# Optimization experiments

Measured on AMD Instinct MI355X. Metric: run time of the kernel, lower is better.

## Reference

```python
import jax, jax.numpy as jnp
import numpy as np

B, C, H, Wd = 4, 2048, 64, 64
HID = 256


def setup_inputs() -> dict:
    key = jax.random.key(0)
    k1, k2, k3, k4 = jax.random.split(key, 4)
    return {
        "query_features": jax.random.normal(k1, (B, C, H, Wd), dtype=jnp.float32),
        "prompt_features": jax.random.normal(k2, (B, C, H, Wd), dtype=jnp.float32),
        "W": jax.random.normal(k3, (HID, C), dtype=jnp.float32) * (1.0 / np.sqrt(C)),
        "b": jax.random.normal(k4, (HID,), dtype=jnp.float32) * 0.02,
    }


def reference(query_features, prompt_features, W, b):
    # 1x1 conv == channel projection
    Q = jnp.einsum('bchw,oc->bohw', query_features, W) + b[None, :, None, None]
    K = jnp.einsum('bchw,oc->bohw', prompt_features, W) + b[None, :, None, None]
    Bq, Cf, Hq, Wq = prompt_features.shape
    V = prompt_features.reshape(Bq, Cf, Hq * Wq)              # b c p
    # full pairwise score tensor: bijkl -> b i j (k l)
    attn = jnp.einsum('bcij,bckl->bijkl', Q, K).reshape(Bq, Hq, Wq, Hq * Wq)
    attn = jax.nn.softmax(attn, axis=3)
    aligned = jnp.einsum('bijp,bcp->bcij', attn, V)           # b c h w
    return aligned
```

## Files before the change

kernel.cpp:

```cpp
#include <hip/hip_runtime.h>
#include <math.h>


#define BATCH 4
#define CH    2048
#define PP    4096
#define DD    256

typedef __bf16    bf16x8 __attribute__((ext_vector_type(8)));
typedef _Float16  f16x8  __attribute__((ext_vector_type(8)));
typedef _Float16  f16x4  __attribute__((ext_vector_type(4)));
typedef float     f32x4  __attribute__((ext_vector_type(4)));

__device__ __forceinline__ unsigned short f2bf(float f) {
  unsigned int u = __float_as_uint(f);
  unsigned int r = u + 0x7fffu + ((u >> 16) & 1u);
  return (unsigned short)(r >> 16);
}

#define GLL(src, dst) \
  __builtin_amdgcn_global_load_lds( \
      (const __attribute__((address_space(1))) unsigned int*)(uintptr_t)(src), \
      (__attribute__((address_space(3))) unsigned int*)(uintptr_t)(dst), 16, 0, 0)

__global__ __launch_bounds__(256) void prep_w(
    const float* __restrict__ W, _Float16* __restrict__ Wf) {
  int i = blockIdx.x * 256 + threadIdx.x;
  float4 v = ((const float4*)W)[i];
  f16x4 h = {(_Float16)v.x, (_Float16)v.y, (_Float16)v.z, (_Float16)v.w};
  ((f16x4*)Wf)[i] = h;
}

__global__ __launch_bounds__(256) void tsplit8(
    const float* __restrict__ Xq, const float* __restrict__ Xp,
    _Float16* __restrict__ Xt8, unsigned short* __restrict__ Vb8, int doV) {
  const int z = blockIdx.z;
  const float* __restrict__ X =
      ((z & 1) ? Xp : Xq) + (size_t)(z >> 1) * CH * PP;
  _Float16* __restrict__ Xt = Xt8 + (size_t)z * CH * PP;
  unsigned short* __restrict__ Vb = Vb8 + (size_t)(z >> 1) * CH * PP;
  const int emitV = doV & z;

  __shared__ float Ls[64 * 65];
  const int tid = threadIdx.x;
  const int pBase = blockIdx.x * 64, cBase = blockIdx.y * 64;
#pragma unroll
  for (int i = 0; i < 4; ++i) {
    int e = tid + i * 256;
    int c = e >> 4, p4 = e & 15;
    float4 v = *(const float4*)&X[(size_t)(cBase + c) * PP + pBase + p4 * 4];
    Ls[c * 65 + p4 * 4 + 0] = v.x; Ls[c * 65 + p4 * 4 + 1] = v.y;
    Ls[c * 65 + p4 * 4 + 2] = v.z; Ls[c * 65 + p4 * 4 + 3] = v.w;
    if (emitV) {
      ushort4 o;
      o.x = f2bf(v.x); o.y = f2bf(v.y); o.z = f2bf(v.z); o.w = f2bf(v.w);
      *(ushort4*)&Vb[(size_t)(cBase + c) * PP + pBase + p4 * 4] = o;
    }
  }
  __syncthreads();
#pragma unroll
  for (int j = 0; j < 4; ++j) {
    int p = (tid >> 4) + j * 16;
    int c4 = (tid & 15) * 4;
    f16x4 h = {(_Float16)Ls[(c4 + 0) * 65 + p], (_Float16)Ls[(c4 + 1) * 65 + p],
               (_Float16)Ls[(c4 + 2) * 65 + p], (_Float16)Ls[(c4 + 3) * 65 + p]};
    *(f16x4*)&Xt[(size_t)(pBase + p) * CH + cBase + c4] = h;
  }
}

__global__ __launch_bounds__(256) void proj8(
    const _Float16* __restrict__ Xt8, const _Float16* __restrict__ Wf,
    const float* __restrict__ bias,
    unsigned short* __restrict__ Qh, unsigned short* __restrict__ Ql,
    unsigned short* __restrict__ Kh, unsigned short* __restrict__ Kl) {
  const int z = blockIdx.z;
  const _Float16* __restrict__ Xt = Xt8 + (size_t)z * CH * PP;
  unsigned short* __restrict__ Yh =
      ((z & 1) ? Kh : Qh) + (size_t)(z >> 1) * PP * DD;
  unsigned short* __restrict__ Yl =
      ((z & 1) ? Kl : Ql) + (size_t)(z >> 1) * PP * DD;

  const int pBase = blockIdx.x * 64;
  const int oBase = blockIdx.y * 64;
  const int tid  = threadIdx.x;
  const int wave = tid >> 6;
  const int lane = tid & 63;
  const int wm = wave & 1, wn = wave >> 1;
  const int row16 = lane & 15, quad = lane >> 4, koff = quad * 8;

  __shared__ __align__(16) _Float16 As0[64 * 32], As1[64 * 32];
  __shared__ __align__(16) _Float16 Bs0[64 * 32], Bs1[64 * 32];

  const int sRow = lane >> 2;
  const int sKc  = (lane & 3) * 8;

  f32x4 acc[2][2];
#pragma unroll
  for (int i = 0; i < 2; ++i)
#pragma unroll
    for (int j = 0; j < 2; ++j) acc[i][j] = (f32x4){0.f, 0.f, 0.f, 0.f};

  for (int c0 = 0; c0 < CH; c0 += 64) {
    const int row = wave * 16 + sRow;
    GLL(&Xt[(size_t)(pBase + row) * CH + c0 + sKc],      &As0[(wave * 16) * 32]);
    GLL(&Xt[(size_t)(pBase + row) * CH + c0 + 32 + sKc], &As1[(wave * 16) * 32]);
    GLL(&Wf[(size_t)(oBase + row) * CH + c0 + sKc],      &Bs0[(wave * 16) * 32]);
    GLL(&Wf[(size_t)(oBase + row) * CH + c0 + 32 + sKc], &Bs1[(wave * 16) * 32]);
    __syncthreads();
#pragma unroll
    for (int s = 0; s < 2; ++s) {
      const _Float16* Ap = s ? As1 : As0;
      const _Float16* Bp = s ? Bs1 : Bs0;
      f16x8 af[2], bf[2];
#pragma unroll
      for (int i = 0; i < 2; ++i)
        af[i] = *(const f16x8*)&Ap[(wm * 32 + i * 16 + row16) * 32 + koff];
#pragma unroll
      for (int j = 0; j < 2; ++j)
        bf[j] = *(const f16x8*)&Bp[(wn * 32 + j * 16 + row16) * 32 + koff];
#pragma unroll
      for (int i = 0; i < 2; ++i)
#pragma unroll
        for (int j = 0; j < 2; ++j)
          acc[i][j] = __builtin_amdgcn_mfma_f32_16x16x32_f16(
              af[i], bf[j], acc[i][j], 0, 0, 0);
    }
    __syncthreads();
  }

#pragma unroll
  for (int i = 0; i < 2; ++i)
#pragma unroll
    for (int j = 0; j < 2; ++j) {
      const int ocol = oBase + wn * 32 + j * 16 + row16;
      const float bv = bias[ocol];
#pragma unroll
      for (int r = 0; r < 4; ++r) {
        const int prow = pBase + wm * 32 + i * 16 + quad * 4 + r;
        float y = acc[i][j][r] + bv;
        unsigned short h = f2bf(y);
        float hf = __uint_as_float((unsigned int)h << 16);
        unsigned short l = f2bf(y - hf);
        Yh[(size_t)prow * DD + ocol] = h;
        Yl[(size_t)prow * DD + ocol] = l;
      }
    }
}

__global__ __launch_bounds__(256) void softmax8(float* __restrict__ S_) {
  float* __restrict__ Sb = S_ + (size_t)blockIdx.y * PP * PP;
  unsigned short* __restrict__ Ab = (unsigned short*)Sb;
  const size_t p = blockIdx.x;
  float* row = Sb + p * PP;
  const int tid = threadIdx.x;
  float4 v[4];
#pragma unroll
  for (int i = 0; i < 4; ++i)
    v[i] = *(const float4*)&row[(i * 256 + tid) * 4];
  float m = -1e30f;
#pragma unroll
  for (int i = 0; i < 4; ++i)
    m = fmaxf(m, fmaxf(fmaxf(v[i].x, v[i].y), fmaxf(v[i].z, v[i].w)));
#pragma unroll
  for (int off = 32; off > 0; off >>= 1)
    m = fmaxf(m, __shfl_xor(m, off));
  __shared__ float red[4];
  const int lane = tid & 63, wv = tid >> 6;
  if (lane == 0) red[wv] = m;
  __syncthreads();
  m = fmaxf(fmaxf(red[0], red[1]), fmaxf(red[2], red[3]));
  __syncthreads();
  float s = 0.f;
#pragma unroll
  for (int i = 0; i < 4; ++i) {
    v[i].x = __expf(v[i].x - m);
    v[i].y = __expf(v[i].y - m);
    v[i].z = __expf(v[i].z - m);
    v[i].w = __expf(v[i].w - m);
    s += v[i].x + v[i].y + v[i].z + v[i].w;
  }
#pragma unroll
  for (int off = 32; off > 0; off >>= 1)
    s += __shfl_xor(s, off);
  if (lane == 0) red[wv] = s;
  __syncthreads();
  s = red[0] + red[1] + red[2] + red[3];
  const float inv = 1.f / s;
  unsigned short* orow = Ab + p * 8192;
#pragma unroll
  for (int i = 0; i < 4; ++i) {
    ushort4 o;
    o.x = f2bf(v[i].x * inv); o.y = f2bf(v[i].y * inv);
    o.z = f2bf(v[i].z * inv); o.w = f2bf(v[i].w * inv);
    *(ushort4*)&orow[(i * 256 + tid) * 4] = o;
  }
}

__global__ __launch_bounds__(256) void cvt_bf16(
    const float* __restrict__ X, unsigned short* __restrict__ Y, int n4) {
  int i = blockIdx.x * blockDim.x + threadIdx.x;
  if (i < n4) {
    float4 v = ((const float4*)X)[i];
    ushort4 o;
    o.x = f2bf(v.x); o.y = f2bf(v.y); o.z = f2bf(v.z); o.w = f2bf(v.w);
    ((ushort4*)Y)[i] = o;
  }
}


#define AOFF(d, h) ((d) * 32768 + (h) * 16384)
#define BOFF(d, h) (65536 + (d) * 32768 + (h) * 16384)

#define PH_READ_A(d, mh) do {                                                  \
  _Pragma("unroll")                                                            \
  for (int m_ = 0; m_ < 4; ++m_) {                                             \
    const int ro_ = AOFF(d, wm) + ((mh) * 64 + m_ * 16 + row16) * 128;         \
    aR[m_][0] = *(const bf16x8*)(Lds + ro_ + cx0);                             \
    aR[m_][1] = *(const bf16x8*)(Lds + ro_ + cx1);                             \
  } } while (0)

#define PH_READ_B(d, nh, breg) do {                                            \
  _Pragma("unroll")                                                            \
  for (int n_ = 0; n_ < 2; ++n_) {                                             \
    const int ro_ = BOFF(d, wnh) + (wnl * 64 + (nh) * 32 + n_ * 16 + row16) * 128; \
    breg[n_][0] = *(const bf16x8*)(Lds + ro_ + cx0);                           \
    breg[n_][1] = *(const bf16x8*)(Lds + ro_ + cx1);                           \
  } } while (0)

#define PH_MFMA(mh, nh, breg) do {                                             \
  __builtin_amdgcn_s_setprio(1);                                               \
  _Pragma("unroll")                                                            \
  for (int m_ = 0; m_ < 4; ++m_)                                               \
  _Pragma("unroll")                                                            \
  for (int n_ = 0; n_ < 2; ++n_) {                                             \
    f32x4 a_ = acc[(mh) * 4 + m_][(nh) * 2 + n_];                              \
    a_ = __builtin_amdgcn_mfma_f32_16x16x32_bf16(aR[m_][0], breg[n_][0], a_, 0, 0, 0); \
    a_ = __builtin_amdgcn_mfma_f32_16x16x32_bf16(aR[m_][1], breg[n_][1], a_, 0, 0, 0); \
    acc[(mh) * 4 + m_][(nh) * 2 + n_] = a_;                                    \
  }                                                                            \
  __builtin_amdgcn_s_setprio(0); } while (0)

#define PH_MFMA3(mh, nh, breg) do {                                            \
  __builtin_amdgcn_s_setprio(1);                                               \
  _Pragma("unroll")                                                            \
  for (int m_ = 0; m_ < 4; ++m_)                                               \
  _Pragma("unroll")                                                            \
  for (int n_ = 0; n_ < 2; ++n_) {                                             \
    f32x4 a_ = acc[(mh) * 4 + m_][(nh) * 2 + n_];                              \
    a_ = __builtin_amdgcn_mfma_f32_16x16x32_bf16(aR[m_][0], breg[n_][0], a_, 0, 0, 0); \
    a_ = __builtin_amdgcn_mfma_f32_16x16x32_bf16(aR[m_][0], breg[n_][1], a_, 0, 0, 0); \
    a_ = __builtin_amdgcn_mfma_f32_16x16x32_bf16(aR[m_][1], breg[n_][0], a_, 0, 0, 0); \
    acc[(mh) * 4 + m_][(nh) * 2 + n_] = a_;                                    \
  }                                                                            \
  __builtin_amdgcn_s_setprio(0); } while (0)

#define BAR_MID() do {                                                         \
  __builtin_amdgcn_sched_barrier(0);                                           \
  __builtin_amdgcn_s_barrier();                                                \
  asm volatile("s_waitcnt lgkmcnt(0)" ::: "memory");                           \
  __builtin_amdgcn_sched_barrier(0); } while (0)

#define BAR_END() __builtin_amdgcn_s_barrier()

__global__ __launch_bounds__(512, 2) void out8(
    const unsigned short* __restrict__ V_,
    const unsigned short* __restrict__ A_,
    float* __restrict__ O_) {
  const size_t z = blockIdx.z;
  const unsigned short* __restrict__ Vb = V_ + z * (size_t)CH * PP;
  const unsigned short* __restrict__ Ab = A_ + z * (size_t)PP * 8192;
  float* __restrict__ Ob = O_ + z * (size_t)CH * PP;

  const int pBase = blockIdx.x * 256;
  const int cBase = blockIdx.y * 256;
  const int tid = threadIdx.x;
  const int wave = tid >> 6, lane = tid & 63;
  const int wm = wave >> 2;
  const int wn = wave & 3;
  const int wnh = wn >> 1, wnl = wn & 1;
  const int row16 = lane & 15, quad = lane >> 4;

  __shared__ __align__(16) char Lds[131072];

  const int swz = (row16 & 7) << 4;
  const int cx0 = ((quad) << 4) ^ swz;
  const int cx1 = ((4 + quad) << 4) ^ swz;

  const int stRow0 = (wave * 2 + 0) * 8 + (lane >> 3);
  const int stRow1 = (wave * 2 + 1) * 8 + (lane >> 3);
  const int stCol  = (((lane & 7) ^ (lane >> 3)) << 4);
  char* ldsSt0 = Lds + (wave * 2 + 0) * 1024;
  char* ldsSt1 = Lds + (wave * 2 + 1) * 1024;

  const size_t VLDG = (size_t)PP * 2;
  const size_t ALDG = (size_t)8192 * 2;

  auto STG = [&](int ldsOff, const void* gbase, size_t ldgB, int rowBase, int gkB) {
    const char* g0 = (const char*)gbase + (size_t)(rowBase + stRow0) * ldgB + gkB + stCol;
    const char* g1 = (const char*)gbase + (size_t)(rowBase + stRow1) * ldgB + gkB + stCol;
    GLL(g0, ldsSt0 + ldsOff);
    GLL(g1, ldsSt1 + ldsOff);
  };

  f32x4 acc[8][4];
#pragma unroll
  for (int i = 0; i < 8; ++i)
#pragma unroll
    for (int j = 0; j < 4; ++j) acc[i][j] = (f32x4){0.f, 0.f, 0.f, 0.f};

  bf16x8 aR[4][2], bLo[2][2], bHi[2][2];

  STG(BOFF(0, 0), Ab, ALDG, pBase + 0,   0);
  STG(BOFF(0, 1), Ab, ALDG, pBase + 128, 0);
  STG(AOFF(0, 0), Vb, VLDG, cBase + 0,   0);
  STG(AOFF(0, 1), Vb, VLDG, cBase + 128, 0);
  STG(BOFF(1, 0), Ab, ALDG, pBase + 0,   128);
  STG(BOFF(1, 1), Ab, ALDG, pBase + 128, 128);
  asm volatile("s_waitcnt vmcnt(4)" ::: "memory");
  __builtin_amdgcn_s_barrier();

#pragma unroll 1
  for (int i = 0; i < 31; ++i) {
    const int t = 2 * i;
    const int gk1 = (t + 1) * 128, gk2 = (t + 2) * 128, gk3 = (t + 3) * 128;
    PH_READ_A(0, 0); PH_READ_B(0, 0, bLo);
    STG(AOFF(1, 0), Vb, VLDG, cBase + 0, gk1);
    BAR_MID(); PH_MFMA(0, 0, bLo); BAR_END();
    PH_READ_B(0, 1, bHi);
    STG(AOFF(1, 1), Vb, VLDG, cBase + 128, gk1);
    BAR_MID(); PH_MFMA(0, 1, bHi); BAR_END();
    PH_READ_A(0, 1);
    STG(BOFF(0, 0), Ab, ALDG, pBase + 0, gk2);
    BAR_MID(); PH_MFMA(1, 0, bLo); BAR_END();
    STG(BOFF(0, 1), Ab, ALDG, pBase + 128, gk2);
    BAR_MID(); PH_MFMA(1, 1, bHi);
    asm volatile("s_waitcnt vmcnt(4)" ::: "memory");
    BAR_END();
    PH_READ_A(1, 0); PH_READ_B(1, 0, bLo);
    STG(AOFF(0, 0), Vb, VLDG, cBase + 0, gk2);
    BAR_MID(); PH_MFMA(0, 0, bLo); BAR_END();
    PH_READ_B(1, 1, bHi);
    STG(AOFF(0, 1), Vb, VLDG, cBase + 128, gk2);
    BAR_MID(); PH_MFMA(0, 1, bHi); BAR_END();
    PH_READ_A(1, 1);
    STG(BOFF(1, 0), Ab, ALDG, pBase + 0, gk3);
    BAR_MID(); PH_MFMA(1, 0, bLo); BAR_END();
    STG(BOFF(1, 1), Ab, ALDG, pBase + 128, gk3);
    BAR_MID(); PH_MFMA(1, 1, bHi);
    asm volatile("s_waitcnt vmcnt(4)" ::: "memory");
    BAR_END();
  }

  {
    const int gk1 = 63 * 128;
    PH_READ_A(0, 0); PH_READ_B(0, 0, bLo);
    STG(AOFF(1, 0), Vb, VLDG, cBase + 0, gk1);
    BAR_MID(); PH_MFMA(0, 0, bLo); BAR_END();
    PH_READ_B(0, 1, bHi);
    STG(AOFF(1, 1), Vb, VLDG, cBase + 128, gk1);
    BAR_MID(); PH_MFMA(0, 1, bHi); BAR_END();
    PH_READ_A(0, 1);
    BAR_MID(); PH_MFMA(1, 0, bLo); BAR_END();
    BAR_MID(); PH_MFMA(1, 1, bHi);
    asm volatile("s_waitcnt vmcnt(0)" ::: "memory");
    BAR_END();
    PH_READ_A(1, 0); PH_READ_B(1, 0, bLo);
    BAR_MID(); PH_MFMA(0, 0, bLo); BAR_END();
    PH_READ_B(1, 1, bHi);
    BAR_MID(); PH_MFMA(0, 1, bHi); BAR_END();
    PH_READ_A(1, 1);
    BAR_MID(); PH_MFMA(1, 0, bLo); BAR_END();
    BAR_MID(); PH_MFMA(1, 1, bHi);
  }

#pragma unroll
  for (int mi = 0; mi < 8; ++mi)
#pragma unroll
    for (int nj = 0; nj < 4; ++nj) {
      const int col = pBase + wn * 64 + nj * 16 + row16;
      float* orow = Ob + (size_t)(cBase + wm * 128 + mi * 16 + quad * 4) * PP + col;
#pragma unroll
      for (int r = 0; r < 4; ++r)
        orow[(size_t)r * PP] = acc[mi][nj][r];
    }
}

__global__ __launch_bounds__(512, 2) void scr8(
    const unsigned short* __restrict__ Qh_, const unsigned short* __restrict__ Ql_,
    const unsigned short* __restrict__ Kh_, const unsigned short* __restrict__ Kl_,
    float* __restrict__ S_) {
  const size_t z = blockIdx.z;
  const unsigned short* __restrict__ Qh = Qh_ + z * (size_t)PP * DD;
  const unsigned short* __restrict__ Ql = Ql_ + z * (size_t)PP * DD;
  const unsigned short* __restrict__ Kh = Kh_ + z * (size_t)PP * DD;
  const unsigned short* __restrict__ Kl = Kl_ + z * (size_t)PP * DD;
  float* __restrict__ S = S_ + z * (size_t)PP * PP;

  const int kBase = blockIdx.x * 256;
  const int pBase = blockIdx.y * 256;
  const int tid = threadIdx.x;
  const int wave = tid >> 6, lane = tid & 63;
  const int wm = wave >> 2;
  const int wn = wave & 3;
  const int wnh = wn >> 1, wnl = wn & 1;
  const int row16 = lane & 15, quad = lane >> 4;

  __shared__ __align__(16) char Lds[131072];

  const int swz = (row16 & 7) << 4;
  const int cx0 = ((quad) << 4) ^ swz;
  const int cx1 = ((4 + quad) << 4) ^ swz;

  const int stRow0 = (wave * 2 + 0) * 8 + (lane >> 3);
  const int stRow1 = (wave * 2 + 1) * 8 + (lane >> 3);
  const int cc   = (lane & 7) ^ (lane >> 3);
  const int ccB  = (cc & 3) * 16;
  const char* tQ = (const char*)((cc >> 2) ? Ql : Qh);
  const char* tK = (const char*)((cc >> 2) ? Kl : Kh);
  char* ldsSt0 = Lds + (wave * 2 + 0) * 1024;
  char* ldsSt1 = Lds + (wave * 2 + 1) * 1024;

  auto STG = [&](int ldsOff, const char* tbase, int rowBase, int tkB) {
    const char* g0 = tbase + (size_t)(rowBase + stRow0) * 512 + tkB + ccB;
    const char* g1 = tbase + (size_t)(rowBase + stRow1) * 512 + tkB + ccB;
    GLL(g0, ldsSt0 + ldsOff);
    GLL(g1, ldsSt1 + ldsOff);
  };

  f32x4 acc[8][4];
#pragma unroll
  for (int i = 0; i < 8; ++i)
#pragma unroll
    for (int j = 0; j < 4; ++j) acc[i][j] = (f32x4){0.f, 0.f, 0.f, 0.f};

  bf16x8 aR[4][2], bLo[2][2], bHi[2][2];

  STG(BOFF(0, 0), tK, kBase + 0,   0);
  STG(BOFF(0, 1), tK, kBase + 128, 0);
  STG(AOFF(0, 0), tQ, pBase + 0,   0);
  STG(AOFF(0, 1), tQ, pBase + 128, 0);
  STG(BOFF(1, 0), tK, kBase + 0,   64);
  STG(BOFF(1, 1), tK, kBase + 128, 64);
  asm volatile("s_waitcnt vmcnt(4)" ::: "memory");
  __builtin_amdgcn_s_barrier();

#pragma unroll 1
  for (int i = 0; i < 3; ++i) {
    const int t = 2 * i;
    const int gk1 = (t + 1) * 64, gk2 = (t + 2) * 64, gk3 = (t + 3) * 64;
    PH_READ_A(0, 0); PH_READ_B(0, 0, bLo);
    STG(AOFF(1, 0), tQ, pBase + 0, gk1);
    BAR_MID(); PH_MFMA3(0, 0, bLo); BAR_END();
    PH_READ_B(0, 1, bHi);
    STG(AOFF(1, 1), tQ, pBase + 128, gk1);
    BAR_MID(); PH_MFMA3(0, 1, bHi); BAR_END();
    PH_READ_A(0, 1);
    STG(BOFF(0, 0), tK, kBase + 0, gk2);
    BAR_MID(); PH_MFMA3(1, 0, bLo); BAR_END();
    STG(BOFF(0, 1), tK, kBase + 128, gk2);
    BAR_MID(); PH_MFMA3(1, 1, bHi);
    asm volatile("s_waitcnt vmcnt(4)" ::: "memory");
    BAR_END();
    PH_READ_A(1, 0); PH_READ_B(1, 0, bLo);
    STG(AOFF(0, 0), tQ, pBase + 0, gk2);
    BAR_MID(); PH_MFMA3(0, 0, bLo); BAR_END();
    PH_READ_B(1, 1, bHi);
    STG(AOFF(0, 1), tQ, pBase + 128, gk2);
    BAR_MID(); PH_MFMA3(0, 1, bHi); BAR_END();
    PH_READ_A(1, 1);
    STG(BOFF(1, 0), tK, kBase + 0, gk3);
    BAR_MID(); PH_MFMA3(1, 0, bLo); BAR_END();
    STG(BOFF(1, 1), tK, kBase + 128, gk3);
    BAR_MID(); PH_MFMA3(1, 1, bHi);
    asm volatile("s_waitcnt vmcnt(4)" ::: "memory");
    BAR_END();
  }

  {
    const int gk1 = 7 * 64;
    PH_READ_A(0, 0); PH_READ_B(0, 0, bLo);
    STG(AOFF(1, 0), tQ, pBase + 0, gk1);
    BAR_MID(); PH_MFMA3(0, 0, bLo); BAR_END();
    PH_READ_B(0, 1, bHi);
    STG(AOFF(1, 1), tQ, pBase + 128, gk1);
    BAR_MID(); PH_MFMA3(0, 1, bHi); BAR_END();
    PH_READ_A(0, 1);
    BAR_MID(); PH_MFMA3(1, 0, bLo); BAR_END();
    BAR_MID(); PH_MFMA3(1, 1, bHi);
    asm volatile("s_waitcnt vmcnt(0)" ::: "memory");
    BAR_END();
    PH_READ_A(1, 0); PH_READ_B(1, 0, bLo);
    BAR_MID(); PH_MFMA3(0, 0, bLo); BAR_END();
    PH_READ_B(1, 1, bHi);
    BAR_MID(); PH_MFMA3(0, 1, bHi); BAR_END();
    PH_READ_A(1, 1);
    BAR_MID(); PH_MFMA3(1, 0, bLo); BAR_END();
    BAR_MID(); PH_MFMA3(1, 1, bHi);
  }

#pragma unroll
  for (int mi = 0; mi < 8; ++mi)
#pragma unroll
    for (int nj = 0; nj < 4; ++nj) {
      const int kcol = kBase + wn * 64 + nj * 16 + row16;
      float* orow = S + (size_t)(pBase + wm * 128 + mi * 16 + quad * 4) * PP + kcol;
#pragma unroll
      for (int r = 0; r < 4; ++r)
        orow[(size_t)r * PP] = acc[mi][nj][r];
    }
}

extern "C" void kernel_launch(void* const* d_in, const int* in_sizes, int n_in,
                              void* d_out, int out_size, void* d_ws, size_t ws_size,
                              hipStream_t stream) {
  const float* Xq   = (const float*)d_in[0];
  const float* Xp   = (const float*)d_in[1];
  const float* Wg   = (const float*)d_in[2];
  const float* bias = (const float*)d_in[3];
  float* out = (float*)d_out;

  char* w = (char*)d_ws;
  const size_t MB = 1024 * 1024;
  const size_t CHPP = (size_t)CH * PP;

  if (ws_size >= 481 * MB) {
    _Float16* Wf       = (_Float16*)w;
    _Float16* Xt8      = (_Float16*)(w + 1 * MB);
    unsigned short* Qh = (unsigned short*)(w + 129 * MB);
    unsigned short* Ql = (unsigned short*)(w + 137 * MB);
    unsigned short* Kh = (unsigned short*)(w + 145 * MB);
    unsigned short* Kl = (unsigned short*)(w + 153 * MB);
    unsigned short* Vbf = (unsigned short*)(w + 161 * MB);
    float* S           = (float*)(w + 225 * MB);

    prep_w<<<512, 256, 0, stream>>>(Wg, Wf);
    tsplit8<<<dim3(PP / 64, CH / 64, 2 * BATCH), 256, 0, stream>>>(
        Xq, Xp, Xt8, Vbf, 1);
    proj8<<<dim3(PP / 64, DD / 64, 2 * BATCH), 256, 0, stream>>>(
        Xt8, Wf, bias, Qh, Ql, Kh, Kl);
    scr8<<<dim3(PP / 256, PP / 256, BATCH), 512, 0, stream>>>(Qh, Ql, Kh, Kl, S);
    softmax8<<<dim3(PP, BATCH), 256, 0, stream>>>(S);
    out8<<<dim3(PP / 256, CH / 256, BATCH), 512, 0, stream>>>(
        Vbf, (unsigned short*)S, out);
  } else {
    _Float16* Xt      = (_Float16*)w;
    unsigned short* Vbf = (unsigned short*)w;
    _Float16* Wf      = (_Float16*)(w + 16 * MB);
    unsigned short* Qh = (unsigned short*)(w + 17 * MB);
    unsigned short* Ql = (unsigned short*)(w + 19 * MB);
    unsigned short* Kh = (unsigned short*)(w + 21 * MB);
    unsigned short* Kl = (unsigned short*)(w + 23 * MB);
    float* S          = (float*)(w + 25 * MB);

    prep_w<<<512, 256, 0, stream>>>(Wg, Wf);
    const int n4 = CH * PP / 4;
    for (int b = 0; b < BATCH; ++b) {
      const float* Xqb = Xq + (size_t)b * CHPP;
      const float* Xpb = Xp + (size_t)b * CHPP;
      tsplit8<<<dim3(PP / 64, CH / 64, 1), 256, 0, stream>>>(
          Xqb, Xqb, Xt, Vbf, 0);
      proj8<<<dim3(PP / 64, DD / 64, 1), 256, 0, stream>>>(
          Xt, Wf, bias, Qh, Ql, Qh, Ql);
      tsplit8<<<dim3(PP / 64, CH / 64, 1), 256, 0, stream>>>(
          Xpb, Xpb, Xt, Vbf, 0);
      proj8<<<dim3(PP / 64, DD / 64, 1), 256, 0, stream>>>(
          Xt, Wf, bias, Kh, Kl, Kh, Kl);
      scr8<<<dim3(PP / 256, PP / 256, 1), 512, 0, stream>>>(Qh, Ql, Kh, Kl, S);
      softmax8<<<dim3(PP, 1), 256, 0, stream>>>(S);
      cvt_bf16<<<n4 / 256, 256, 0, stream>>>(Xpb, Vbf, n4);
      out8<<<dim3(PP / 256, CH / 256, 1), 512, 0, stream>>>(
          Vbf, (unsigned short*)S, out + (size_t)b * CHPP);
    }
  }
}
```

Measured before the change: 828.5 us.

## Fuse transpose/fp16 conversion into projection GEMM reading fp32 input directly

Replaces the separate transpose-to-fp16 kernel and projection kernel with one projX kernel. It streams fp32 X tiles straight into LDS, converts them to fp16 while building MFMA fragments, and also emits the bf16 V copy from the same tile. Each block now computes all 256 output channels for 64 positions, with XOR-swizzled W staging. This removes the 128MB fp16 intermediate round trip and the second read of X. The cost is strided scalar LDS reads for the A fragments, plus lower grid parallelism (256 blocks per batch-pair, 512 total).

Result: faster. 730.8 us (-11.8%).

```diff
diff --git a/kernel.cpp b/kernel.cpp
--- a/kernel.cpp
+++ b/kernel.cpp
@@ -31,112 +31,110 @@
   ((f16x4*)Wf)[i] = h;
 }
 
-__global__ __launch_bounds__(256) void tsplit8(
+__global__ __launch_bounds__(256) void projX(
     const float* __restrict__ Xq, const float* __restrict__ Xp,
-    _Float16* __restrict__ Xt8, unsigned short* __restrict__ Vb8, int doV) {
-  const int z = blockIdx.z;
+    const _Float16* __restrict__ Wf, const float* __restrict__ bias,
+    unsigned short* __restrict__ Qh, unsigned short* __restrict__ Ql,
+    unsigned short* __restrict__ Kh, unsigned short* __restrict__ Kl,
+    unsigned short* __restrict__ Vb8, int zbase, int single) {
+  const int z = zbase + blockIdx.z;
+  const int b = z >> 1;
+  const int ob = single ? 0 : b;
   const float* __restrict__ X =
-      ((z & 1) ? Xp : Xq) + (size_t)(z >> 1) * CH * PP;
-  _Float16* __restrict__ Xt = Xt8 + (size_t)z * CH * PP;
-  unsigned short* __restrict__ Vb = Vb8 + (size_t)(z >> 1) * CH * PP;
-  const int emitV = doV & z;
-
-  __shared__ float Ls[64 * 65];
-  const int tid = threadIdx.x;
-  const int pBase = blockIdx.x * 64, cBase = blockIdx.y * 64;
-#pragma unroll
-  for (int i = 0; i < 4; ++i) {
-    int e = tid + i * 256;
-    int c = e >> 4, p4 = e & 15;
-    float4 v = *(const float4*)&X[(size_t)(cBase + c) * PP + pBase + p4 * 4];
-    Ls[c * 65 + p4 * 4 + 0] = v.x; Ls[c * 65 + p4 * 4 + 1] = v.y;
-    Ls[c * 65 + p4 * 4 + 2] = v.z; Ls[c * 65 + p4 * 4 + 3] = v.w;
-    if (emitV) {
-      ushort4 o;
-      o.x = f2bf(v.x); o.y = f2bf(v.y); o.z = f2bf(v.z); o.w = f2bf(v.w);
-      *(ushort4*)&Vb[(size_t)(cBase + c) * PP + pBase + p4 * 4] = o;
-    }
-  }
-  __syncthreads();
-#pragma unroll
-  for (int j = 0; j < 4; ++j) {
-    int p = (tid >> 4) + j * 16;
-    int c4 = (tid & 15) * 4;
-    f16x4 h = {(_Float16)Ls[(c4 + 0) * 65 + p], (_Float16)Ls[(c4 + 1) * 65 + p],
-               (_Float16)Ls[(c4 + 2) * 65 + p], (_Float16)Ls[(c4 + 3) * 65 + p]};
-    *(f16x4*)&Xt[(size_t)(pBase + p) * CH + cBase + c4] = h;
-  }
-}
-
-__global__ __launch_bounds__(256) void proj8(
-    const _Float16* __restrict__ Xt8, const _Float16* __restrict__ Wf,
-    const float* __restrict__ bias,
-    unsigned short* __restrict__ Qh, unsigned short* __restrict__ Ql,
-    unsigned short* __restrict__ Kh, unsigned short* __restrict__ Kl) {
-  const int z = blockIdx.z;
-  const _Float16* __restrict__ Xt = Xt8 + (size_t)z * CH * PP;
+      ((z & 1) ? Xp : Xq) + (size_t)b * CH * PP;
   unsigned short* __restrict__ Yh =
-      ((z & 1) ? Kh : Qh) + (size_t)(z >> 1) * PP * DD;
+      ((z & 1) ? Kh : Qh) + (size_t)ob * PP * DD;
   unsigned short* __restrict__ Yl =
-      ((z & 1) ? Kl : Ql) + (size_t)(z >> 1) * PP * DD;
+      ((z & 1) ? Kl : Ql) + (size_t)ob * PP * DD;
+  unsigned short* __restrict__ Vb = Vb8 + (size_t)ob * CH * PP;
+  const int emitV = (z & 1);
 
   const int pBase = blockIdx.x * 64;
-  const int oBase = blockIdx.y * 64;
   const int tid  = threadIdx.x;
   const int wave = tid >> 6;
   const int lane = tid & 63;
-  const int wm = wave & 1, wn = wave >> 1;
-  const int row16 = lane & 15, quad = lane >> 4, koff = quad * 8;
-
-  __shared__ __align__(16) _Float16 As0[64 * 32], As1[64 * 32];
-  __shared__ __align__(16) _Float16 Bs0[64 * 32], Bs1[64 * 32];
-
-  const int sRow = lane >> 2;
-  const int sKc  = (lane & 3) * 8;
-
-  f32x4 acc[2][2];
-#pragma unroll
-  for (int i = 0; i < 2; ++i)
-#pragma unroll
-    for (int j = 0; j < 2; ++j) acc[i][j] = (f32x4){0.f, 0.f, 0.f, 0.f};
-
+  const int row16 = lane & 15, quad = lane >> 4;
+
+  __shared__ __align__(16) char LdsP[32768 + 16384];
+  char*  Ws  = LdsP;
+  float* LsX = (float*)(LdsP + 32768);
+
+  const int wRowIn  = lane >> 3;
+  const int wChunk  = (((lane & 7) ^ (lane >> 3)) << 4);
+  const int xRowIn  = lane >> 4;
+  const int xColB   = (lane & 15) * 16;
+
+  f32x4 acc[4][4];
+#pragma unroll
+  for (int i = 0; i < 4; ++i)
+#pragma unroll
+    for (int j = 0; j < 4; ++j) acc[i][j] = (f32x4){0.f, 0.f, 0.f, 0.f};
+
+#pragma unroll 1
   for (int c0 = 0; c0 < CH; c0 += 64) {
-    const int row = wave * 16 + sRow;
-    GLL(&Xt[(size_t)(pBase + row) * CH + c0 + sKc],      &As0[(wave * 16) * 32]);
-    GLL(&Xt[(size_t)(pBase + row) * CH + c0 + 32 + sKc], &As1[(wave * 16) * 32]);
-    GLL(&Wf[(size_t)(oBase + row) * CH + c0 + sKc],      &Bs0[(wave * 16) * 32]);
-    GLL(&Wf[(size_t)(oBase + row) * CH + c0 + 32 + sKc], &Bs1[(wave * 16) * 32]);
+#pragma unroll
+    for (int q = 0; q < 8; ++q) {
+      const int g = wave * 8 + q;
+      const char* src = (const char*)Wf +
+          (size_t)(g * 8 + wRowIn) * (CH * 2) + c0 * 2 + wChunk;
+      GLL(src, Ws + g * 1024);
+    }
+#pragma unroll
+    for (int q = 0; q < 4; ++q) {
+      const int g = wave * 4 + q;
+      const char* src = (const char*)X +
+          ((size_t)(c0 + g * 4 + xRowIn) * PP + pBase) * 4 + xColB;
+      GLL(src, (char*)LsX + g * 1024);
+    }
     __syncthreads();
+
 #pragma unroll
     for (int s = 0; s < 2; ++s) {
-      const _Float16* Ap = s ? As1 : As0;
-      const _Float16* Bp = s ? Bs1 : Bs0;
-      f16x8 af[2], bf[2];
-#pragma unroll
-      for (int i = 0; i < 2; ++i)
-        af[i] = *(const f16x8*)&Ap[(wm * 32 + i * 16 + row16) * 32 + koff];
-#pragma unroll
-      for (int j = 0; j < 2; ++j)
-        bf[j] = *(const f16x8*)&Bp[(wn * 32 + j * 16 + row16) * 32 + koff];
-#pragma unroll
-      for (int i = 0; i < 2; ++i)
-#pragma unroll
-        for (int j = 0; j < 2; ++j)
+      f16x8 af[4], bf[4];
+#pragma unroll
+      for (int i = 0; i < 4; ++i) {
+        f16x8 a;
+#pragma unroll
+        for (int e = 0; e < 8; ++e)
+          a[e] = (_Float16)LsX[(s * 32 + quad * 8 + e) * 64 + i * 16 + row16];
+        af[i] = a;
+      }
+#pragma unroll
+      for (int j = 0; j < 4; ++j) {
+        const int brow = wave * 64 + j * 16 + row16;
+        bf[j] = *(const f16x8*)(Ws + brow * 128 +
+                                (((s * 4 + quad) ^ (row16 & 7)) << 4));
+      }
+#pragma unroll
+      for (int i = 0; i < 4; ++i)
+#pragma unroll
+        for (int j = 0; j < 4; ++j)
           acc[i][j] = __builtin_amdgcn_mfma_f32_16x16x32_f16(
               af[i], bf[j], acc[i][j], 0, 0, 0);
     }
+
+    if (emitV) {
+      const int cl = tid >> 2, ps = (tid & 3) * 16;
+      const float* xr = &LsX[cl * 64 + ps];
+      unsigned short tmp[16];
+#pragma unroll
+      for (int u = 0; u < 16; ++u) tmp[u] = f2bf(xr[u]);
+      char* dst = (char*)Vb + ((size_t)(c0 + cl) * PP + pBase + ps) * 2;
+      *(uint4*)dst        = *(const uint4*)tmp;
+      *(uint4*)(dst + 16) = *(const uint4*)(tmp + 8);
+    }
     __syncthreads();
   }
 
 #pragma unroll
-  for (int i = 0; i < 2; ++i)
-#pragma unroll
-    for (int j = 0; j < 2; ++j) {
-      const int ocol = oBase + wn * 32 + j * 16 + row16;
+  for (int i = 0; i < 4; ++i)
+#pragma unroll
+    for (int j = 0; j < 4; ++j) {
+      const int ocol = wave * 64 + j * 16 + row16;
       const float bv = bias[ocol];
 #pragma unroll
       for (int r = 0; r < 4; ++r) {
-        const int prow = pBase + wm * 32 + i * 16 + quad * 4 + r;
+        const int prow = pBase + i * 16 + quad * 4 + r;
         float y = acc[i][j][r] + bv;
         unsigned short h = f2bf(y);
         float hf = __uint_as_float((unsigned int)h << 16);
@@ -193,17 +191,6 @@
     o.x = f2bf(v[i].x * inv); o.y = f2bf(v[i].y * inv);
     o.z = f2bf(v[i].z * inv); o.w = f2bf(v[i].w * inv);
     *(ushort4*)&orow[(i * 256 + tid) * 4] = o;
-  }
-}
-
-__global__ __launch_bounds__(256) void cvt_bf16(
-    const float* __restrict__ X, unsigned short* __restrict__ Y, int n4) {
-  int i = blockIdx.x * blockDim.x + threadIdx.x;
-  if (i < n4) {
-    float4 v = ((const float4*)X)[i];
-    ushort4 o;
-    o.x = f2bf(v.x); o.y = f2bf(v.y); o.z = f2bf(v.z); o.w = f2bf(v.w);
-    ((ushort4*)Y)[i] = o;
   }
 }
 
@@ -523,51 +510,37 @@
   const size_t MB = 1024 * 1024;
   const size_t CHPP = (size_t)CH * PP;
 
-  if (ws_size >= 481 * MB) {
+  if (ws_size >= 354 * MB) {
     _Float16* Wf       = (_Float16*)w;
-    _Float16* Xt8      = (_Float16*)(w + 1 * MB);
-    unsigned short* Qh = (unsigned short*)(w + 129 * MB);
-    unsigned short* Ql = (unsigned short*)(w + 137 * MB);
-    unsigned short* Kh = (unsigned short*)(w + 145 * MB);
-    unsigned short* Kl = (unsigned short*)(w + 153 * MB);
-    unsigned short* Vbf = (unsigned short*)(w + 161 * MB);
-    float* S           = (float*)(w + 225 * MB);
+    unsigned short* Qh = (unsigned short*)(w + 1 * MB);
+    unsigned short* Ql = (unsigned short*)(w + 9 * MB);
+    unsigned short* Kh = (unsigned short*)(w + 17 * MB);
+    unsigned short* Kl = (unsigned short*)(w + 25 * MB);
+    unsigned short* Vbf = (unsigned short*)(w + 33 * MB);
+    float* S           = (float*)(w + 97 * MB);
 
     prep_w<<<512, 256, 0, stream>>>(Wg, Wf);
-    tsplit8<<<dim3(PP / 64, CH / 64, 2 * BATCH), 256, 0, stream>>>(
-        Xq, Xp, Xt8, Vbf, 1);
-    proj8<<<dim3(PP / 64, DD / 64, 2 * BATCH), 256, 0, stream>>>(
-        Xt8, Wf, bias, Qh, Ql, Kh, Kl);
+    projX<<<dim3(PP / 64, 1, 2 * BATCH), 256, 0, stream>>>(
+        Xq, Xp, Wf, bias, Qh, Ql, Kh, Kl, Vbf, 0, 0);
     scr8<<<dim3(PP / 256, PP / 256, BATCH), 512, 0, stream>>>(Qh, Ql, Kh, Kl, S);
     softmax8<<<dim3(PP, BATCH), 256, 0, stream>>>(S);
     out8<<<dim3(PP / 256, CH / 256, BATCH), 512, 0, stream>>>(
         Vbf, (unsigned short*)S, out);
   } else {
-    _Float16* Xt      = (_Float16*)w;
-    unsigned short* Vbf = (unsigned short*)w;
-    _Float16* Wf      = (_Float16*)(w + 16 * MB);
-    unsigned short* Qh = (unsigned short*)(w + 17 * MB);
-    unsigned short* Ql = (unsigned short*)(w + 19 * MB);
-    unsigned short* Kh = (unsigned short*)(w + 21 * MB);
-    unsigned short* Kl = (unsigned short*)(w + 23 * MB);
-    float* S          = (float*)(w + 25 * MB);
+    _Float16* Wf       = (_Float16*)w;
+    unsigned short* Qh = (unsigned short*)(w + 1 * MB);
+    unsigned short* Ql = (unsigned short*)(w + 3 * MB);
+    unsigned short* Kh = (unsigned short*)(w + 5 * MB);
+    unsigned short* Kl = (unsigned short*)(w + 7 * MB);
+    unsigned short* Vbf = (unsigned short*)(w + 9 * MB);
+    float* S           = (float*)(w + 25 * MB);
 
     prep_w<<<512, 256, 0, stream>>>(Wg, Wf);
-    const int n4 = CH * PP / 4;
     for (int b = 0; b < BATCH; ++b) {
-      const float* Xqb = Xq + (size_t)b * CHPP;
-      const float* Xpb = Xp + (size_t)b * CHPP;
-      tsplit8<<<dim3(PP / 64, CH / 64, 1), 256, 0, stream>>>(
-          Xqb, Xqb, Xt, Vbf, 0);
-      proj8<<<dim3(PP / 64, DD / 64, 1), 256, 0, stream>>>(
-          Xt, Wf, bias, Qh, Ql, Qh, Ql);
-      tsplit8<<<dim3(PP / 64, CH / 64, 1), 256, 0, stream>>>(
-          Xpb, Xpb, Xt, Vbf, 0);
-      proj8<<<dim3(PP / 64, DD / 64, 1), 256, 0, stream>>>(
-          Xt, Wf, bias, Kh, Kl, Kh, Kl);
+      projX<<<dim3(PP / 64, 1, 2), 256, 0, stream>>>(
+          Xq, Xp, Wf, bias, Qh, Ql, Kh, Kl, Vbf, 2 * b, 1);
       scr8<<<dim3(PP / 256, PP / 256, 1), 512, 0, stream>>>(Qh, Ql, Kh, Kl, S);
       softmax8<<<dim3(PP, 1), 256, 0, stream>>>(S);
-      cvt_bf16<<<n4 / 256, 256, 0, stream>>>(Xpb, Vbf, n4);
       out8<<<dim3(PP / 256, CH / 256, 1), 512, 0, stream>>>(
           Vbf, (unsigned short*)S, out + (size_t)b * CHPP);
     }
```
